# Kernel tuning notes

Measured on AMD Instinct MI355X. Metric: run time of the kernel, lower is better.

The kernel has to match this reference:

```python
import jax, jax.numpy as jnp
import numpy as np
from jax import lax

DROPOUT_RATE = 0.1  # config['dropout']


def setup_inputs() -> dict:
    key = jax.random.key(0)
    kx, kl, kwi, kwh = jax.random.split(key, 4)
    B, T, D, H = 64, 2048, 256, 256
    datamat = jax.random.normal(kx, (B, T, D), dtype=jnp.float32)
    datalens = jax.random.randint(kl, (B,), 1, T + 1, dtype=jnp.int32)
    # OptimizedLSTMCell params: combined input/hidden kernels, gate order (i, f, g, o)
    s_i = 1.0 / np.sqrt(D)
    s_h = 1.0 / np.sqrt(H)
    Wi = jax.random.uniform(kwi, (D, 4 * H), jnp.float32, -s_i, s_i)
    Wh = jax.random.uniform(kwh, (H, 4 * H), jnp.float32, -s_h, s_h)
    b = jnp.zeros((4 * H,), dtype=jnp.float32)
    return {"datamat": datamat, "Wi": Wi, "Wh": Wh, "b": b, "datalens": datalens}


def _dropout(x, rate):
    # training=True dropout with a fixed key (deterministic reference)
    keep = jax.random.bernoulli(jax.random.key(42), 1.0 - rate, x.shape)
    return jnp.where(keep, x / (1.0 - rate), jnp.zeros_like(x))


def _lstm_forward(x, Wi, Wh, b, datalens):
    # x: [B, T, D]
    B, T, D = x.shape
    H = Wh.shape[0]

    def step(carry, xt):
        c, h = carry
        z = xt @ Wi + h @ Wh + b  # [B, 4H], gate order i, f, g, o
        i, f, g, o = jnp.split(z, 4, axis=-1)
        c_new = jax.nn.sigmoid(f) * c + jax.nn.sigmoid(i) * jnp.tanh(g)
        h_new = jax.nn.sigmoid(o) * jnp.tanh(c_new)
        return (c_new, h_new), (c_new, h_new)

    c0 = jnp.zeros((B, H), dtype=x.dtype)
    h0 = jnp.zeros((B, H), dtype=x.dtype)
    _, (cs, hs) = lax.scan(step, (c0, h0), jnp.swapaxes(x, 0, 1))  # [T, B, H] each
    outputs = jnp.swapaxes(hs, 0, 1)  # [B, T, H]
    # flax nn.RNN with seq_lengths + return_carry: select carry at t = len-1 per batch
    idx = jnp.clip(datalens.astype(jnp.int32) - 1, 0, T - 1)  # [B]
    bidx = jnp.arange(B)
    c_last = cs[idx, bidx]  # [B, H]
    h_last = hs[idx, bidx]  # [B, H]
    return (c_last, h_last), outputs


def reference(datamat, Wi, Wh, b, datalens):
    x = _dropout(datamat, DROPOUT_RATE)
    out_carry, outputs = _lstm_forward(x, Wi, Wh, b, datalens)
    return (out_carry, outputs)
```

## Files before the change

kernel.cpp:

```cpp
#include <hip/hip_runtime.h>


typedef __attribute__((ext_vector_type(8))) short short8;
typedef __attribute__((ext_vector_type(4))) float floatx4;
typedef __attribute__((ext_vector_type(4))) int int4v;
typedef __attribute__((ext_vector_type(4))) unsigned short us4;

#define LOG2E 1.44269504088896f

__device__ __forceinline__ unsigned short f2bf(float f) {
  unsigned int u = __float_as_uint(f);
  u = u + 0x7fffu + ((u >> 16) & 1u);
  return (unsigned short)(u >> 16);
}
__device__ __forceinline__ float fexp2(float x) { return __builtin_amdgcn_exp2f(x); }
__device__ __forceinline__ float frcp(float x) { return __builtin_amdgcn_rcpf(x); }

__device__ __forceinline__ unsigned int tf_bits(unsigned int x0, unsigned int x1) {
  const unsigned int K0 = 0u, K1 = 42u;
  const unsigned int KX = K0 ^ K1 ^ 0x1BD11BDAu;
  x0 += K0; x1 += K1;
#define TF_R(r) { x0 += x1; x1 = (x1 << (r)) | (x1 >> (32 - (r))); x1 ^= x0; }
  TF_R(13) TF_R(15) TF_R(26) TF_R(6)   x0 += K1; x1 += KX + 1u;
  TF_R(17) TF_R(29) TF_R(16) TF_R(24)  x0 += KX; x1 += K0 + 2u;
  TF_R(13) TF_R(15) TF_R(26) TF_R(6)   x0 += K0; x1 += K1 + 3u;
  TF_R(17) TF_R(29) TF_R(16) TF_R(24)  x0 += K1; x1 += KX + 4u;
  TF_R(13) TF_R(15) TF_R(26) TF_R(6)   x0 += KX; x1 += K0 + 5u;
#undef TF_R
  return x0 ^ x1;
}

__global__ __launch_bounds__(256) void k_dropout(const float* __restrict__ x,
                                                 unsigned short* __restrict__ xd) {
  const unsigned int base = (blockIdx.x * 256u + threadIdx.x) * 4u;
  const float4 xv = *reinterpret_cast<const float4*>(x + base);
  const float xs[4] = {xv.x, xv.y, xv.z, xv.w};
  us4 o;
#pragma unroll
  for (int j = 0; j < 4; ++j) {
    const unsigned int bits = tf_bits(0u, base + (unsigned int)j);
    const float u = __uint_as_float((bits >> 9) | 0x3f800000u) - 1.0f;
    const float v = (u < 0.9f) ? (xs[j] / 0.9f) : 0.0f;
    o[j] = f2bf(v);
  }
  *reinterpret_cast<us4*>(xd + base) = o;
}

__global__ __launch_bounds__(256) void k_pack_wi(const float* __restrict__ wi,
                                                 unsigned short* __restrict__ wit) {
  __shared__ float tile[32][33];
  const int k0 = blockIdx.x * 32, n0 = blockIdx.y * 32;
  const int tx = threadIdx.x & 31, ty = threadIdx.x >> 5;
#pragma unroll
  for (int i = 0; i < 4; ++i)
    tile[ty + i * 8][tx] = wi[(k0 + ty + i * 8) * 1024 + n0 + tx];
  __syncthreads();
#pragma unroll
  for (int i = 0; i < 4; ++i)
    wit[(n0 + ty + i * 8) * 256 + k0 + tx] = f2bf(tile[tx][ty + i * 8]);
}

__global__ __launch_bounds__(256) void k_colscale(const float* __restrict__ wh,
                                                  float* __restrict__ dq,
                                                  float* __restrict__ qs) {
  __shared__ float red[256];
  const int t = threadIdx.x;
  const int n = blockIdx.x * 16 + (t & 15);
  const int kg = t >> 4;
  float m = 0.f;
#pragma unroll
  for (int i = 0; i < 16; ++i)
    m = fmaxf(m, fabsf(wh[(kg * 16 + i) * 1024 + n]));
  red[t] = m;
  __syncthreads();
  if (t < 16) {
    const int nn = blockIdx.x * 16 + t;
    float mm = red[t];
#pragma unroll
    for (int j = 1; j < 16; ++j) mm = fmaxf(mm, red[t + j * 16]);
    const float s = (mm > 0.f) ? mm : 1.f;
    const float gsc[4] = {LOG2E, -LOG2E, 2.f * LOG2E, LOG2E};
    dq[nn] = (s / 16129.0f) * gsc[nn >> 8];
    qs[nn] = 127.0f / s;
  }
}

__global__ __launch_bounds__(256) void k_pack_wh_i8(const float* __restrict__ wh,
                                                    const float* __restrict__ qs,
                                                    signed char* __restrict__ wq) {
  const int tid = blockIdx.x * 256 + threadIdx.x;
  const int j = tid & 15, l = (tid >> 4) & 63, kt = (tid >> 10) & 3, ntg = tid >> 12;
  const int k = kt * 64 + ((l >> 4) << 4) + j;
  const int n = ntg * 16 + (l & 15);
  float v = rintf(wh[k * 1024 + n] * qs[n]);
  v = fminf(fmaxf(v, -127.f), 127.f);
  wq[tid] = (signed char)(int)v;
}

__global__ __launch_bounds__(256) void k_gemm_x(const unsigned short* __restrict__ xd,
                                                const unsigned short* __restrict__ wit,
                                                const float* __restrict__ bias,
                                                unsigned short* __restrict__ xp) {
  __shared__ unsigned short SH[20480];
  const int tid = threadIdx.x;
  const int lane = tid & 63;
  const int wv = tid >> 6;
  const int wm = wv >> 1, wn = wv & 1;
  const int m0 = blockIdx.x * 128;
  const int y = blockIdx.y;

  const int srow = tid >> 1, sseg = tid & 1;
  const unsigned short* gA = xd + (m0 + srow) * 256 + sseg * 16;
  const int nsrc = ((srow >> 5) << 8) + y * 32 + (srow & 31);
  const unsigned short* gB = wit + nsrc * 256 + sseg * 16;
  const int soff = srow * 40 + sseg * 16;

  const floatx4 zero4 = {0.f, 0.f, 0.f, 0.f};
  floatx4 acc[4][4];
#pragma unroll
  for (int i = 0; i < 4; ++i)
#pragma unroll
    for (int j = 0; j < 4; ++j) acc[i][j] = zero4;

  short8 ra0 = *(const short8*)(gA);
  short8 ra1 = *(const short8*)(gA + 8);
  short8 rb0 = *(const short8*)(gB);
  short8 rb1 = *(const short8*)(gB + 8);
  *(short8*)&SH[soff] = ra0;
  *(short8*)&SH[soff + 8] = ra1;
  *(short8*)&SH[10240 + soff] = rb0;
  *(short8*)&SH[10240 + soff + 8] = rb1;
  __syncthreads();

  const int frow = (lane & 15) * 40 + ((lane >> 4) << 3);
#pragma unroll 1
  for (int kt = 0; kt < 8; ++kt) {
    const int boff = (kt & 1) * 5120;
    if (kt < 7) {
      ra0 = *(const short8*)(gA + (kt + 1) * 32);
      ra1 = *(const short8*)(gA + (kt + 1) * 32 + 8);
      rb0 = *(const short8*)(gB + (kt + 1) * 32);
      rb1 = *(const short8*)(gB + (kt + 1) * 32 + 8);
    }
    short8 af[4], bfv[4];
#pragma unroll
    for (int mt = 0; mt < 4; ++mt)
      af[mt] = *(const short8*)&SH[boff + (wm * 64 + mt * 16) * 40 + frow];
#pragma unroll
    for (int nt = 0; nt < 4; ++nt)
      bfv[nt] = *(const short8*)&SH[10240 + boff + (wn * 64 + nt * 16) * 40 + frow];
#pragma unroll
    for (int mt = 0; mt < 4; ++mt)
#pragma unroll
      for (int nt = 0; nt < 4; ++nt)
        acc[mt][nt] = __builtin_amdgcn_mfma_f32_16x16x32_bf16(af[mt], bfv[nt], acc[mt][nt], 0, 0, 0);
    if (kt < 7) {
      const int noff = (boff ^ 5120);
      *(short8*)&SH[noff + soff] = ra0;
      *(short8*)&SH[noff + soff + 8] = ra1;
      *(short8*)&SH[10240 + noff + soff] = rb0;
      *(short8*)&SH[10240 + noff + soff + 8] = rb1;
    }
    __syncthreads();
  }

  const float gsc[4] = {LOG2E, -LOG2E, 2.f * LOG2E, LOG2E};
  float bv[4], gv[4];
#pragma unroll
  for (int nt = 0; nt < 4; ++nt) {
    const int gate = wn * 2 + (nt >> 1);
    bv[nt] = bias[(gate << 8) + y * 32 + ((nt & 1) << 4) + (lane & 15)];
    gv[nt] = gsc[gate];
  }

  __syncthreads();
#pragma unroll
  for (int mt = 0; mt < 4; ++mt) {
#pragma unroll
    for (int nt = 0; nt < 4; ++nt) {
      const int jj = wn * 64 + nt * 16 + (lane & 15);
#pragma unroll
      for (int q = 0; q < 4; ++q) {
        const int row = wm * 64 + mt * 16 + ((lane >> 4) << 2) + q;
        SH[row * 132 + jj] = f2bf((acc[mt][nt][q] + bv[nt]) * gv[nt]);
      }
    }
  }
  __syncthreads();

#pragma unroll
  for (int k = 0; k < 16; ++k) {
    const int pi = k * 256 + tid;
    const int row = pi >> 5, u = pi & 31;
    us4 o = {SH[row * 132 + u], SH[row * 132 + 32 + u],
             SH[row * 132 + 64 + u], SH[row * 132 + 96 + u]};
    const int m = m0 + row;
    *(us4*)(xp + ((size_t)(m & 2047) * 64 + (m >> 11)) * 1024 +
            (size_t)(y * 32 + u) * 4) = o;
  }
}

__global__ __launch_bounds__(512, 2) void k_lstm(const unsigned short* __restrict__ xp,
                                                 const signed char* __restrict__ wq,
                                                 const float* __restrict__ dq,
                                                 const int* __restrict__ lens,
                                                 float* __restrict__ out) {
  __shared__ __align__(16) signed char As[8192];

  const int tid = threadIdx.x, lane = tid & 63, v = tid >> 6;
  const int wg = blockIdx.x, b0 = wg * 2;

  const int4v zacc = {0, 0, 0, 0};
  ((int4v*)As)[tid] = zacc;

  int4v w[4][2][4];
#pragma unroll
  for (int g = 0; g < 4; ++g)
#pragma unroll
    for (int p = 0; p < 2; ++p)
#pragma unroll
      for (int kt = 0; kt < 4; ++kt) {
        const int ntg = g * 16 + v * 2 + p;
        w[g][p][kt] = *(const int4v*)(wq + (size_t)(((ntg * 4 + kt) * 64 + lane)) * 16);
      }

  const int r = (lane >> 4) & 1;
  const int ph = lane >> 5;
  const int u = v * 32 + ph * 16 + (lane & 15);

  float dq0 = dq[u], dq1 = dq[256 + u], dq2 = dq[512 + u], dq3 = dq[768 + u];
  const int lenm = lens[b0 + r] - 1;
  float c = 0.f, ckeep = 0.f, hkeep = 0.f;

  const signed char* AsR = As + lane * 16;
  signed char* AsW = As + ((u >> 6) * 1024 + (((u >> 4) & 3) * 16 + r * 4) * 16 + (u & 15));

  const char* xpb = (const char*)xp;
  unsigned int xoff = ((unsigned int)(b0 + r) * 1024u + (unsigned int)u * 4u) * 2u;
  char* outb = (char*)(out + 32768);
  unsigned int ooff = ((unsigned int)(b0 + r) * 524288u + (unsigned int)u) * 4u;

  uint2 xc = *(const uint2*)(xpb + xoff);
  xoff += 131072u;

  __syncthreads();

#define GATES(XPAIR, WOFF0, WOFF1)                                              \
  {                                                                             \
    const float xi = __uint_as_float(XPAIR.x << 16);                            \
    const float xf = __uint_as_float(XPAIR.x & 0xffff0000u);                    \
    const float xg = __uint_as_float(XPAIR.y << 16);                            \
    const float xo = __uint_as_float(XPAIR.y & 0xffff0000u);                    \
    const int ai = ph ? acc[0][1][0] : acc[0][0][0];                            \
    const int af_ = ph ? acc[1][1][0] : acc[1][0][0];                           \
    const int ag = ph ? acc[2][1][0] : acc[2][0][0];                            \
    const int ao = ph ? acc[3][1][0] : acc[3][0][0];                            \
    const float zi = fminf(fmaf((float)ai, dq0, xi), 28.85f);                   \
    const float zf = fmaf((float)af_, dq1, xf);                                 \
    const float zg = fminf(fmaf((float)ag, dq2, xg), 57.71f);                   \
    const float zo = fminf(fmaf((float)ao, dq3, xo), 28.85f);                   \
    const float ei = fexp2(zi);                                                 \
    const float e2g = fexp2(zg);                                                \
    const float ef = fexp2(zf);                                                 \
    const float eo = fexp2(zo);                                                 \
    const float p1 = ei * (e2g - 1.f) * frcp((ei + 1.f) * (e2g + 1.f));         \
    const float cn = fmaf(frcp(1.f + ef), c, p1);                               \
    c = cn;                                                                     \
    const float e2c = fexp2(fminf(cn, 15.f) * (2.f * LOG2E));                   \
    const float h = eo * (e2c - 1.f) * frcp((eo + 1.f) * (e2c + 1.f));          \
    const float hm = fmaf(h, 127.f, 12582912.f);                                \
    AsW[WOFF0] = (signed char)__float_as_uint(hm);                              \
    AsW[WOFF1] = (signed char)__float_as_uint(hm);                              \
    *(float*)(outb + ooff) = h;                                                 \
    ooff += 1024u;                                                              \
    if (t_ == lenm) { ckeep = cn; hkeep = h; }                                  \
  }

#define MFMA_BLOCK(O0, O1, O2, O3)                                              \
  int4v acc[4][2];                                                              \
  {                                                                             \
    const int4v a0 = *(const int4v*)(AsR + (O0));                               \
    const int4v a1 = *(const int4v*)(AsR + (O1));                               \
    const int4v a2 = *(const int4v*)(AsR + (O2));                               \
    const int4v a3 = *(const int4v*)(AsR + (O3));                               \
    _Pragma("unroll") for (int g = 0; g < 4; ++g)                               \
    _Pragma("unroll") for (int p = 0; p < 2; ++p) {                             \
      acc[g][p] = __builtin_amdgcn_mfma_i32_16x16x64_i8(a0, w[g][p][0], zacc, 0, 0, 0); \
      acc[g][p] = __builtin_amdgcn_mfma_i32_16x16x64_i8(a1, w[g][p][1], acc[g][p], 0, 0, 0); \
      acc[g][p] = __builtin_amdgcn_mfma_i32_16x16x64_i8(a2, w[g][p][2], acc[g][p], 0, 0, 0); \
      acc[g][p] = __builtin_amdgcn_mfma_i32_16x16x64_i8(a3, w[g][p][3], acc[g][p], 0, 0, 0); \
    }                                                                           \
  }

#pragma unroll 1
  for (int it = 0; it < 1024; ++it) {
    {
      const int t_ = 2 * it;
      const uint2 xn = *(const uint2*)(xpb + xoff);
      xoff += 131072u;
      MFMA_BLOCK(0, 1024, 2048, 3072)
      GATES(xc, 4096, 4224)
      xc = xn;
      __syncthreads();
    }
    {
      const int t_ = 2 * it + 1;
      const uint2 xn = *(const uint2*)(xpb + xoff);
      xoff += 131072u;
      MFMA_BLOCK(4096, 5120, 6144, 7168)
      GATES(xc, 0, 128)
      xc = xn;
      __syncthreads();
    }
  }
#undef GATES
#undef MFMA_BLOCK

  out[(size_t)(b0 + r) * 256 + u] = ckeep;
  out[16384 + (size_t)(b0 + r) * 256 + u] = hkeep;
}

extern "C" void kernel_launch(void* const* d_in, const int* in_sizes, int n_in,
                              void* d_out, int out_size, void* d_ws, size_t ws_size,
                              hipStream_t stream) {
  (void)in_sizes; (void)n_in; (void)out_size; (void)ws_size;
  const float* x = (const float*)d_in[0];
  const float* wi = (const float*)d_in[1];
  const float* wh = (const float*)d_in[2];
  const float* bias = (const float*)d_in[3];
  const int* lens = (const int*)d_in[4];
  float* out = (float*)d_out;

  char* ws = (char*)d_ws;
  unsigned short* xd = (unsigned short*)ws;
  unsigned short* xp = (unsigned short*)(ws + 67108864ull);
  unsigned short* wit = (unsigned short*)(ws + 335544320ull);
  float* dq = (float*)(ws + 336068608ull);
  float* qs = (float*)(ws + 336072704ull);
  signed char* wqb = (signed char*)(ws + 336076800ull);

  k_pack_wi<<<dim3(8, 32), 256, 0, stream>>>(wi, wit);
  k_colscale<<<64, 256, 0, stream>>>(wh, dq, qs);
  k_pack_wh_i8<<<1024, 256, 0, stream>>>(wh, qs, wqb);
  k_dropout<<<32768, 256, 0, stream>>>(x, xd);
  k_gemm_x<<<dim3(1024, 8), 256, 0, stream>>>(xd, wit, bias, xp);
  k_lstm<<<32, 512, 0, stream>>>(xp, wqb, dq, lens, out);
}
```

Before: 1.542 ms.

## Fuse input GEMM and LSTM recurrence into one kernel with chunk flags

Merges the input-projection GEMM and the recurrent LSTM kernel into a single launch. The first 32 blocks run the recurrence, and the remaining blocks compute time-chunked GEMM tiles that signal completion through global atomic counters. Recurrence blocks wait on the flag for the next 128-step chunk before consuming it, so the GEMM overlaps with the serial scan and the launch gap goes away. This relies on all 32 recurrence blocks staying resident alongside the GEMM blocks, which risks deadlock if they are not scheduled. It also adds spin-wait overhead and shrinks the GEMM tile to 128x128 with 512 threads.

```diff
diff --git a/kernel.cpp b/kernel.cpp
--- a/kernel.cpp
+++ b/kernel.cpp
@@ -97,118 +97,113 @@
   wq[tid] = (signed char)(int)v;
 }
 
-__global__ __launch_bounds__(256) void k_gemm_x(const unsigned short* __restrict__ xd,
-                                                const unsigned short* __restrict__ wit,
-                                                const float* __restrict__ bias,
-                                                unsigned short* __restrict__ xp) {
-  __shared__ unsigned short SH[20480];
-  const int tid = threadIdx.x;
-  const int lane = tid & 63;
-  const int wv = tid >> 6;
-  const int wm = wv >> 1, wn = wv & 1;
-  const int m0 = blockIdx.x * 128;
-  const int y = blockIdx.y;
-
-  const int srow = tid >> 1, sseg = tid & 1;
-  const unsigned short* gA = xd + (m0 + srow) * 256 + sseg * 16;
-  const int nsrc = ((srow >> 5) << 8) + y * 32 + (srow & 31);
-  const unsigned short* gB = wit + nsrc * 256 + sseg * 16;
-  const int soff = srow * 40 + sseg * 16;
-
-  const floatx4 zero4 = {0.f, 0.f, 0.f, 0.f};
-  floatx4 acc[4][4];
-#pragma unroll
-  for (int i = 0; i < 4; ++i)
-#pragma unroll
-    for (int j = 0; j < 4; ++j) acc[i][j] = zero4;
-
-  short8 ra0 = *(const short8*)(gA);
-  short8 ra1 = *(const short8*)(gA + 8);
-  short8 rb0 = *(const short8*)(gB);
-  short8 rb1 = *(const short8*)(gB + 8);
-  *(short8*)&SH[soff] = ra0;
-  *(short8*)&SH[soff + 8] = ra1;
-  *(short8*)&SH[10240 + soff] = rb0;
-  *(short8*)&SH[10240 + soff + 8] = rb1;
-  __syncthreads();
-
-  const int frow = (lane & 15) * 40 + ((lane >> 4) << 3);
+__global__ __launch_bounds__(512, 2) void k_fused(
+    const unsigned short* __restrict__ xd, const unsigned short* __restrict__ wit,
+    const float* __restrict__ bias, unsigned short* __restrict__ xp,
+    const signed char* __restrict__ wq, const float* __restrict__ dq,
+    const int* __restrict__ lens, float* __restrict__ out,
+    unsigned int* __restrict__ flags) {
+  __shared__ __align__(16) unsigned short SH[45056];
+
+  const int tid = threadIdx.x, lane = tid & 63;
+
+  if (blockIdx.x >= 32) {
+    const int gb = (int)blockIdx.x - 32;
+    const int tc = gb >> 9;
+    const int rem = gb & 511;
+    const int b = rem >> 3, y = rem & 7;
+    const int m0 = b * 2048 + tc * 128;
+
+    const int wv = tid >> 6;
+    const int wm = wv >> 2;
+    const int wn = wv & 3;
+    const int srow = tid >> 2, sseg = tid & 3;
+    const unsigned short* gA = xd + (m0 + srow) * 256 + sseg * 8;
+    const int nsrc = ((srow >> 5) << 8) + y * 32 + (srow & 31);
+    const unsigned short* gB = wit + nsrc * 256 + sseg * 8;
+    const int soff = srow * 40 + sseg * 8;
+
+    const floatx4 zero4 = {0.f, 0.f, 0.f, 0.f};
+    floatx4 acc[4][2];
+#pragma unroll
+    for (int i = 0; i < 4; ++i) { acc[i][0] = zero4; acc[i][1] = zero4; }
+
+    short8 ra = *(const short8*)(gA);
+    short8 rb = *(const short8*)(gB);
+    *(short8*)&SH[soff] = ra;
+    *(short8*)&SH[10240 + soff] = rb;
+    __syncthreads();
+
+    const int frow = (lane & 15) * 40 + ((lane >> 4) << 3);
 #pragma unroll 1
-  for (int kt = 0; kt < 8; ++kt) {
-    const int boff = (kt & 1) * 5120;
-    if (kt < 7) {
-      ra0 = *(const short8*)(gA + (kt + 1) * 32);
-      ra1 = *(const short8*)(gA + (kt + 1) * 32 + 8);
-      rb0 = *(const short8*)(gB + (kt + 1) * 32);
-      rb1 = *(const short8*)(gB + (kt + 1) * 32 + 8);
-    }
-    short8 af[4], bfv[4];
+    for (int kt = 0; kt < 8; ++kt) {
+      const int boff = (kt & 1) * 5120;
+      if (kt < 7) {
+        ra = *(const short8*)(gA + (kt + 1) * 32);
+        rb = *(const short8*)(gB + (kt + 1) * 32);
+      }
+      short8 af[4], bfv[2];
+#pragma unroll
+      for (int mt = 0; mt < 4; ++mt)
+        af[mt] = *(const short8*)&SH[boff + (wm * 64 + mt * 16) * 40 + frow];
+#pragma unroll
+      for (int nt = 0; nt < 2; ++nt)
+        bfv[nt] = *(const short8*)&SH[10240 + boff + (wn * 32 + nt * 16) * 40 + frow];
+#pragma unroll
+      for (int mt = 0; mt < 4; ++mt)
+#pragma unroll
+        for (int nt = 0; nt < 2; ++nt)
+          acc[mt][nt] = __builtin_amdgcn_mfma_f32_16x16x32_bf16(af[mt], bfv[nt], acc[mt][nt], 0, 0, 0);
+      if (kt < 7) {
+        const int noff = boff ^ 5120;
+        *(short8*)&SH[noff + soff] = ra;
+        *(short8*)&SH[10240 + noff + soff] = rb;
+      }
+      __syncthreads();
+    }
+
+    const float gsc[4] = {LOG2E, -LOG2E, 2.f * LOG2E, LOG2E};
+    const float gv = gsc[wn];
+    float bv[2];
+#pragma unroll
+    for (int nt = 0; nt < 2; ++nt)
+      bv[nt] = bias[wn * 256 + y * 32 + nt * 16 + (lane & 15)];
+
+    __syncthreads();
 #pragma unroll
     for (int mt = 0; mt < 4; ++mt)
-      af[mt] = *(const short8*)&SH[boff + (wm * 64 + mt * 16) * 40 + frow];
-#pragma unroll
-    for (int nt = 0; nt < 4; ++nt)
-      bfv[nt] = *(const short8*)&SH[10240 + boff + (wn * 64 + nt * 16) * 40 + frow];
-#pragma unroll
-    for (int mt = 0; mt < 4; ++mt)
-#pragma unroll
-      for (int nt = 0; nt < 4; ++nt)
-        acc[mt][nt] = __builtin_amdgcn_mfma_f32_16x16x32_bf16(af[mt], bfv[nt], acc[mt][nt], 0, 0, 0);
-    if (kt < 7) {
-      const int noff = (boff ^ 5120);
-      *(short8*)&SH[noff + soff] = ra0;
-      *(short8*)&SH[noff + soff + 8] = ra1;
-      *(short8*)&SH[10240 + noff + soff] = rb0;
-      *(short8*)&SH[10240 + noff + soff + 8] = rb1;
-    }
+#pragma unroll
+      for (int nt = 0; nt < 2; ++nt) {
+        const int jj = wn * 32 + nt * 16 + (lane & 15);
+#pragma unroll
+        for (int q = 0; q < 4; ++q) {
+          const int row = wm * 64 + mt * 16 + ((lane >> 4) << 2) + q;
+          SH[row * 132 + jj] = f2bf((acc[mt][nt][q] + bv[nt]) * gv);
+        }
+      }
     __syncthreads();
-  }
-
-  const float gsc[4] = {LOG2E, -LOG2E, 2.f * LOG2E, LOG2E};
-  float bv[4], gv[4];
-#pragma unroll
-  for (int nt = 0; nt < 4; ++nt) {
-    const int gate = wn * 2 + (nt >> 1);
-    bv[nt] = bias[(gate << 8) + y * 32 + ((nt & 1) << 4) + (lane & 15)];
-    gv[nt] = gsc[gate];
-  }
-
-  __syncthreads();
-#pragma unroll
-  for (int mt = 0; mt < 4; ++mt) {
-#pragma unroll
-    for (int nt = 0; nt < 4; ++nt) {
-      const int jj = wn * 64 + nt * 16 + (lane & 15);
-#pragma unroll
-      for (int q = 0; q < 4; ++q) {
-        const int row = wm * 64 + mt * 16 + ((lane >> 4) << 2) + q;
-        SH[row * 132 + jj] = f2bf((acc[mt][nt][q] + bv[nt]) * gv[nt]);
-      }
-    }
-  }
-  __syncthreads();
-
-#pragma unroll
-  for (int k = 0; k < 16; ++k) {
-    const int pi = k * 256 + tid;
-    const int row = pi >> 5, u = pi & 31;
-    us4 o = {SH[row * 132 + u], SH[row * 132 + 32 + u],
-             SH[row * 132 + 64 + u], SH[row * 132 + 96 + u]};
-    const int m = m0 + row;
-    *(us4*)(xp + ((size_t)(m & 2047) * 64 + (m >> 11)) * 1024 +
-            (size_t)(y * 32 + u) * 4) = o;
-  }
-}
-
-__global__ __launch_bounds__(512, 2) void k_lstm(const unsigned short* __restrict__ xp,
-                                                 const signed char* __restrict__ wq,
-                                                 const float* __restrict__ dq,
-                                                 const int* __restrict__ lens,
-                                                 float* __restrict__ out) {
-  __shared__ __align__(16) signed char As[8192];
-
-  const int tid = threadIdx.x, lane = tid & 63, v = tid >> 6;
-  const int wg = blockIdx.x, b0 = wg * 2;
+
+#pragma unroll
+    for (int k = 0; k < 8; ++k) {
+      const int pi = k * 512 + tid;
+      const int row = pi >> 5, u = pi & 31;
+      us4 o = {SH[row * 132 + u], SH[row * 132 + 32 + u],
+               SH[row * 132 + 64 + u], SH[row * 132 + 96 + u]};
+      const int m = m0 + row;
+      *(us4*)(xp + ((size_t)(m & 2047) * 64 + (m >> 11)) * 1024 +
+              (size_t)(y * 32 + u) * 4) = o;
+    }
+
+    __threadfence();
+    __syncthreads();
+    if (tid == 0) atomicAdd(&flags[tc], 1u);
+    return;
+  }
+
+  signed char* As = (signed char*)SH;
+
+  const int v = tid >> 6;
+  const int wg = (int)blockIdx.x, b0 = wg * 2;
 
   const int4v zacc = {0, 0, 0, 0};
   ((int4v*)As)[tid] = zacc;
@@ -239,6 +234,12 @@
   unsigned int xoff = ((unsigned int)(b0 + r) * 1024u + (unsigned int)u * 4u) * 2u;
   char* outb = (char*)(out + 32768);
   unsigned int ooff = ((unsigned int)(b0 + r) * 524288u + (unsigned int)u) * 4u;
+
+  if (tid == 0) {
+    while (__hip_atomic_load(&flags[0], __ATOMIC_ACQUIRE, __HIP_MEMORY_SCOPE_AGENT) < 512u)
+      __builtin_amdgcn_s_sleep(8);
+  }
+  __syncthreads();
 
   uint2 xc = *(const uint2*)(xpb + xoff);
   xoff += 131072u;
@@ -294,6 +295,15 @@
 
 #pragma unroll 1
   for (int it = 0; it < 1024; ++it) {
+    if ((it & 63) == 0) {
+      const int ch0 = (it >> 6) + 1;
+      const int ch = ch0 < 15 ? ch0 : 15;
+      if (tid == 0) {
+        while (__hip_atomic_load(&flags[ch], __ATOMIC_ACQUIRE, __HIP_MEMORY_SCOPE_AGENT) < 512u)
+          __builtin_amdgcn_s_sleep(8);
+      }
+      __syncthreads();
+    }
     {
       const int t_ = 2 * it;
       const uint2 xn = *(const uint2*)(xpb + xoff);
@@ -338,11 +348,12 @@
   float* dq = (float*)(ws + 336068608ull);
   float* qs = (float*)(ws + 336072704ull);
   signed char* wqb = (signed char*)(ws + 336076800ull);
-
+  unsigned int* flags = (unsigned int*)(ws + 336338944ull);
+
+  hipMemsetAsync(flags, 0, 64, stream);
   k_pack_wi<<<dim3(8, 32), 256, 0, stream>>>(wi, wit);
   k_colscale<<<64, 256, 0, stream>>>(wh, dq, qs);
   k_pack_wh_i8<<<1024, 256, 0, stream>>>(wh, qs, wqb);
   k_dropout<<<32768, 256, 0, stream>>>(x, xd);
-  k_gemm_x<<<dim3(1024, 8), 256, 0, stream>>>(xd, wit, bias, xp);
-  k_lstm<<<32, 512, 0, stream>>>(xp, wqb, dq, lens, out);
-}
+  k_fused<<<8224, 512, 0, stream>>>(xd, wit, bias, xp, wqb, dq, lens, out, flags);
+}
```

Result: slower. 3.103 ms (+101.3%).
